# Optimization experiments

Measured on AMD Instinct MI355X. Metric: run time of the kernel, lower is better.

The kernel has to match this reference:

```python
import jax, jax.numpy as jnp
import numpy as np

B, S, E, H = 2, 2048, 1024, 16
DH = E // H  # 64


def setup_inputs() -> dict:
    key = jax.random.key(0)
    ks = jax.random.split(key, 9)
    sc = 1.0 / np.sqrt(E)
    return {
        "x": jax.random.normal(ks[0], (B, S, E), dtype=jnp.float32),
        "Wq": jax.random.normal(ks[1], (E, E), dtype=jnp.float32) * sc,
        "bq": jax.random.normal(ks[2], (E,), dtype=jnp.float32) * 0.02,
        "Wk": jax.random.normal(ks[3], (E, E), dtype=jnp.float32) * sc,
        "bk": jax.random.normal(ks[4], (E,), dtype=jnp.float32) * 0.02,
        "Wv": jax.random.normal(ks[5], (E, E), dtype=jnp.float32) * sc,
        "bv": jax.random.normal(ks[6], (E,), dtype=jnp.float32) * 0.02,
        "Wo": jax.random.normal(ks[7], (E, E), dtype=jnp.float32) * sc,
        "bo": jax.random.normal(ks[8], (E,), dtype=jnp.float32) * 0.02,
    }


def reference(x, Wq, bq, Wk, bk, Wv, bv, Wo, bo):
    b, s, e = x.shape
    h, dh = H, e // H
    # NOTE: original torch code does .view(B, H, S, Dh) on the [B, S, E]
    # projection WITHOUT transposing first; we replicate that exact reshape.
    q = (x @ Wq.T + bq).reshape(b, h, s, dh)
    k = (x @ Wk.T + bk).reshape(b, h, s, dh)
    v = (x @ Wv.T + bv).reshape(b, h, s, dh)
    scale = 1.0 / jnp.sqrt(jnp.asarray(dh, dtype=x.dtype))
    scores = jax.nn.softmax(jnp.einsum("bhqd,bhkd->bhqk", q, k) * scale, axis=-1)
    out = jnp.einsum("bhqk,bhkd->bhqd", scores, v)  # [B,H,S,Dh]
    out = out.transpose(0, 2, 1, 3).reshape(b, s, e)  # matches torch transpose(1,2).view
    return out @ Wo.T + bo
```

## Files before the change

### kernel.cpp

```cpp
#include <hip/hip_runtime.h>
#include <hip/hip_bf16.h>
#include <stdint.h>

typedef __bf16 bf16x8 __attribute__((ext_vector_type(8)));
typedef float  f32x4  __attribute__((ext_vector_type(4)));
typedef float  f32x16 __attribute__((ext_vector_type(16)));
typedef __hip_bfloat16 bf16;

__device__ __forceinline__ void gll16(const void* g, void* l) {
    typedef const unsigned int __attribute__((address_space(1)))* gp_t;
    typedef unsigned int __attribute__((address_space(3)))* lp_t;
    __builtin_amdgcn_global_load_lds((gp_t)(g), (lp_t)(l), 16, 0, 0);
}

__device__ __forceinline__ float fexp2(float x) {
#if __has_builtin(__builtin_amdgcn_exp2f)
    return __builtin_amdgcn_exp2f(x);
#else
    float r; asm volatile("v_exp_f32 %0, %1" : "=v"(r) : "v"(x)); return r;
#endif
}

__device__ __forceinline__ float tmax16(const f32x16& v) {
    float a0 = fmaxf(v[0], v[1]),   a1 = fmaxf(v[2], v[3]);
    float a2 = fmaxf(v[4], v[5]),   a3 = fmaxf(v[6], v[7]);
    float a4 = fmaxf(v[8], v[9]),   a5 = fmaxf(v[10], v[11]);
    float a6 = fmaxf(v[12], v[13]), a7 = fmaxf(v[14], v[15]);
    float b0 = fmaxf(a0, a1), b1 = fmaxf(a2, a3);
    float b2 = fmaxf(a4, a5), b3 = fmaxf(a6, a7);
    return fmaxf(fmaxf(b0, b1), fmaxf(b2, b3));
}
__device__ __forceinline__ float tsum16(const f32x16& v) {
    float a0 = v[0] + v[1],   a1 = v[2] + v[3];
    float a2 = v[4] + v[5],   a3 = v[6] + v[7];
    float a4 = v[8] + v[9],   a5 = v[10] + v[11];
    float a6 = v[12] + v[13], a7 = v[14] + v[15];
    float b0 = a0 + a1, b1 = a2 + a3, b2 = a4 + a5, b3 = a6 + a7;
    return (b0 + b1) + (b2 + b3);
}

__global__ __launch_bounds__(256) void prep_convert(
    const float* __restrict__ x,
    const float* __restrict__ wq, const float* __restrict__ wk,
    const float* __restrict__ wv, const float* __restrict__ wo,
    bf16* __restrict__ Xb, bf16* __restrict__ Wcat, bf16* __restrict__ Wob)
{
    int i = blockIdx.x * blockDim.x + threadIdx.x;
    int base = i * 4;
    const float* src; bf16* dst;
    if      (base < 4194304) { src = x  + base;             dst = Xb   + base; }
    else if (base < 5242880) { src = wq + (base - 4194304); dst = Wcat + (base - 4194304); }
    else if (base < 6291456) { src = wk + (base - 5242880); dst = Wcat + 1048576 + (base - 5242880); }
    else if (base < 7340032) { src = wv + (base - 6291456); dst = Wcat + 2097152 + (base - 6291456); }
    else                     { src = wo + (base - 7340032); dst = Wob  + (base - 7340032); }
    float4 v = *(const float4*)src;
    union { bf16 h[4]; ushort4 u; } cv;
    cv.h[0] = __float2bfloat16(v.x);
    cv.h[1] = __float2bfloat16(v.y);
    cv.h[2] = __float2bfloat16(v.z);
    cv.h[3] = __float2bfloat16(v.w);
    *(ushort4*)dst = cv.u;
}

__global__ __launch_bounds__(256, 2) void gemm_qkv(
    const bf16* __restrict__ X, const bf16* __restrict__ Wc,
    const float* __restrict__ bq, const float* __restrict__ bk, const float* __restrict__ bv,
    bf16* __restrict__ Pq, bf16* __restrict__ Pk, bf16* __restrict__ Pv)
{
    __shared__ __align__(16) bf16 Ab[128 * 32];
    __shared__ __align__(16) bf16 Bb[128 * 32];
    const int id = blockIdx.x;
    const int sid = (id & 7) * 96 + (id >> 3);
    const int t = threadIdx.x;
    const int lane = t & 63, w = t >> 6;
    const int lr = lane & 15, lg = lane >> 4;
    const int wr = w >> 1, wc = w & 1;
    const int row0 = (sid / 24) * 128, col0 = (sid % 24) * 128;

    f32x4 acc[4][4] = {};

    const char* Xc  = (const char*)X;
    const char* Wcc = (const char*)Wc;
    char* AbC = (char*)Ab;
    char* BbC = (char*)Bb;
    const int o0 = t * 16, o1 = o0 + 4096;
    const int ldsoff = w * 1024;

    for (int k0 = 0; k0 < 1024; k0 += 32) {
        __syncthreads();
        gll16(Xc  + (size_t)(row0 + (o0 >> 6)) * 2048 + (size_t)k0 * 2 + (o0 & 63), AbC + ldsoff);
        gll16(Wcc + (size_t)(col0 + (o0 >> 6)) * 2048 + (size_t)k0 * 2 + (o0 & 63), BbC + ldsoff);
        gll16(Xc  + (size_t)(row0 + (o1 >> 6)) * 2048 + (size_t)k0 * 2 + (o1 & 63), AbC + 4096 + ldsoff);
        gll16(Wcc + (size_t)(col0 + (o1 >> 6)) * 2048 + (size_t)k0 * 2 + (o1 & 63), BbC + 4096 + ldsoff);
        __syncthreads();
        bf16x8 af[4], bw[4];
        #pragma unroll
        for (int i = 0; i < 4; ++i)
            af[i] = *(const bf16x8*)(AbC + ((wr * 64 + i * 16 + lr) * 32 + lg * 8) * 2);
        #pragma unroll
        for (int j = 0; j < 4; ++j)
            bw[j] = *(const bf16x8*)(BbC + ((wc * 64 + j * 16 + lr) * 32 + lg * 8) * 2);
        #pragma unroll
        for (int i = 0; i < 4; ++i)
            #pragma unroll
            for (int j = 0; j < 4; ++j)
                acc[i][j] = __builtin_amdgcn_mfma_f32_16x16x32_bf16(af[i], bw[j], acc[i][j], 0, 0, 0);
    }

    const int mid = col0 >> 10;
    const float* bias = (mid == 0) ? bq : (mid == 1 ? bk : bv);
    bf16* Out = (mid == 0) ? Pq : (mid == 1 ? Pk : Pv);
    const float scale = (mid == 0) ? 0.125f * 1.44269504f : 1.0f;
    const int nc0 = col0 - (mid << 10) + wc * 64;
    const int mr0 = row0 + wr * 64;
    #pragma unroll
    for (int i = 0; i < 4; ++i)
        #pragma unroll
        for (int j = 0; j < 4; ++j) {
            int cc = nc0 + j * 16 + lr;
            float bsv = bias[cc];
            #pragma unroll
            for (int p = 0; p < 4; ++p) {
                int rr = mr0 + i * 16 + lg * 4 + p;
                Out[(size_t)rr * 1024 + cc] = __float2bfloat16((acc[i][j][p] + bsv) * scale);
            }
        }
}

__global__ __launch_bounds__(256) void transpose_v(const bf16* __restrict__ Pv, bf16* __restrict__ Vt)
{
    __shared__ bf16 tile[64][72];
    const int head = blockIdx.y;
    const int st   = blockIdx.x;
    const bf16* src = Pv + (size_t)head * 131072 + (size_t)st * 4096;
    bf16* dst = Vt + (size_t)head * 131072 + (size_t)st * 64;
    const int t = threadIdx.x;
    const int rr = t >> 2, c0 = (t & 3) * 16;
    #pragma unroll
    for (int u = 0; u < 2; ++u) {
        bf16x8 v = *(const bf16x8*)(src + rr * 64 + c0 + u * 8);
        #pragma unroll
        for (int e = 0; e < 8; ++e) tile[rr][c0 + u * 8 + e] = ((const bf16*)&v)[e];
    }
    __syncthreads();
    #pragma unroll
    for (int u = 0; u < 2; ++u) {
        bf16 ov[8];
        #pragma unroll
        for (int e = 0; e < 8; ++e) {
            int y = u * 8 + e;
            int z = (y & 3) | ((y & 8) >> 1) | ((y & 4) << 1);
            ov[e] = tile[c0 + z][rr];
        }
        *(bf16x8*)(dst + (size_t)rr * 2048 + c0 + u * 8) = *(const bf16x8*)ov;
    }
}

__global__ __launch_bounds__(512, 4) void attn_fwd(
    const bf16* __restrict__ Pq, const bf16* __restrict__ Pk,
    const bf16* __restrict__ Vt, bf16* __restrict__ Of)
{
    __shared__ __align__(16) bf16 Kl[2][128 * 64];
    __shared__ __align__(16) bf16 Vl[2][64 * 128];

    const int blk0 = blockIdx.x;
    const int blk = (blk0 & 7) * 64 + (blk0 >> 3);
    const int head = blk >> 4;
    const int qt = blk & 15;
    const int bb = head >> 4, hh = head & 15;
    const bf16* Qh = Pq + (size_t)head * 131072;
    const char* Khc = (const char*)(Pk + (size_t)head * 131072);
    const char* Vhc = (const char*)(Vt + (size_t)head * 131072);

    const int t = threadIdx.x;
    const int lane = t & 63, w = t >> 6;
    const int qg = w & 3, kh = w >> 2;
    const int ql = lane & 31, hi = lane >> 5;
    const int q0 = qt * 128 + qg * 32;

    bf16x8 qf[4];
    #pragma unroll
    for (int m = 0; m < 4; ++m)
        qf[m] = *(const bf16x8*)(Qh + (size_t)(q0 + ql) * 64 + m * 16 + hi * 8);

    f32x16 acc[2] = {};
    float m_run = -1e30f, l_run = 0.f;

    const int stg_key = t >> 3, stg_ks = t & 7;
    const int stg_d   = t >> 4, stg_vs = t & 15;
    const size_t kgo = (size_t)stg_key * 128 + ((stg_ks ^ (stg_key & 7)) * 16);
    const size_t vgo = (size_t)stg_d * 4096 + ((stg_vs ^ (stg_d & 7)) * 16);
    const int ldst = w * 1024;

#define STAGE(S0, BUF)                                                          \
    {                                                                           \
        char* KB = (char*)(Kl[BUF]);                                            \
        char* VB = (char*)(Vl[BUF]);                                            \
        _Pragma("unroll")                                                       \
        for (int qq = 0; qq < 2; ++qq) {                                        \
            gll16(Khc + (size_t)(S0) * 128 + (size_t)qq * 8192 + kgo,           \
                  KB + qq * 8192 + ldst);                                       \
            gll16(Vhc + (size_t)(S0) * 2 + (size_t)qq * 131072 + vgo,           \
                  VB + qq * 8192 + ldst);                                       \
        }                                                                       \
    }

    STAGE(0, 0);
    STAGE(128, 1);

    int cur = 0;
    for (int s0 = 0; s0 < 2048; s0 += 128) {
        if (s0 < 1920) {
            asm volatile("s_waitcnt vmcnt(4)\n\ts_barrier" ::: "memory");
        } else {
            asm volatile("s_waitcnt vmcnt(0)\n\ts_barrier" ::: "memory");
        }

        const char* KlC = (const char*)(Kl[cur]);
        const char* VlC = (const char*)(Vl[cur]);

        f32x16 sa[2] = {};
        __builtin_amdgcn_s_setprio(1);
        #pragma unroll
        for (int kb = 0; kb < 2; ++kb) {
            int row = kh * 64 + kb * 32 + ql;
            #pragma unroll
            for (int m = 0; m < 4; ++m) {
                int byt = row * 128 + ((32 * m + 16 * hi) ^ ((row & 7) << 4));
                bf16x8 kf = *(const bf16x8*)(KlC + byt);
                sa[kb] = __builtin_amdgcn_mfma_f32_32x32x16_bf16(kf, qf[m], sa[kb], 0, 0, 0);
            }
        }
        __builtin_amdgcn_s_setprio(0);

        float mx = fmaxf(tmax16(sa[0]), tmax16(sa[1]));
        mx = fmaxf(mx, __shfl_xor(mx, 32));

        float mn;
        if (__all(mx - m_run <= 8.0f)) {
            mn = m_run;
        } else {
            mn = fmaxf(m_run, mx);
            float al = fexp2(m_run - mn);
            m_run = mn;
            l_run *= al;
            #pragma unroll
            for (int r = 0; r < 16; ++r) { acc[0][r] *= al; acc[1][r] *= al; }
        }

        #pragma unroll
        for (int kb = 0; kb < 2; ++kb)
            #pragma unroll
            for (int r = 0; r < 16; ++r)
                sa[kb][r] = fexp2(sa[kb][r] - mn);
        float rs = tsum16(sa[0]) + tsum16(sa[1]);
        rs += __shfl_xor(rs, 32);
        l_run += rs;

        __builtin_amdgcn_s_setprio(1);
        #pragma unroll
        for (int sbl = 0; sbl < 4; ++sbl) {
            const int kb = sbl >> 1, par = (sbl & 1) * 8;
            const int sbg = kh * 4 + sbl;
            bf16x8 pa;
            #pragma unroll
            for (int e = 0; e < 8; ++e) pa[e] = (__bf16)sa[kb][par + e];
            #pragma unroll
            for (int db = 0; db < 2; ++db) {
                int row = db * 32 + ql;
                int byt = row * 256 + ((sbg * 32 + hi * 16) ^ ((row & 7) << 4));
                bf16x8 vf = *(const bf16x8*)(VlC + byt);
                acc[db] = __builtin_amdgcn_mfma_f32_32x32x16_bf16(vf, pa, acc[db], 0, 0, 0);
            }
        }
        __builtin_amdgcn_s_setprio(0);

        __builtin_amdgcn_s_barrier();
        if (s0 + 256 < 2048) STAGE(s0 + 256, cur);
        cur ^= 1;
    }
#undef STAGE

    float* cb1 = (float*)Kl;
    float* cb2 = (float*)Vl;
    const int idx = qg * 64 + lane;
    if (kh == 1) {
        #pragma unroll
        for (int r = 0; r < 16; ++r) cb1[idx * 18 + r] = acc[0][r];
        cb1[idx * 18 + 16] = m_run;
        cb1[idx * 18 + 17] = l_run;
        #pragma unroll
        for (int r = 0; r < 16; ++r) cb2[idx * 17 + r] = acc[1][r];
    }
    __syncthreads();
    if (kh == 0) {
        float m1 = cb1[idx * 18 + 16], l1 = cb1[idx * 18 + 17];
        float mN = fmaxf(m_run, m1);
        float a0 = fexp2(m_run - mN), a1 = fexp2(m1 - mN);
        float inv = 1.0f / (l_run * a0 + l1 * a1);
        bf16* orow = Of + (size_t)(bb * 2048 + q0 + ql) * 1024 + hh * 64;
        #pragma unroll
        for (int db = 0; db < 2; ++db)
            #pragma unroll
            for (int g = 0; g < 4; ++g) {
                union { bf16 h[4]; ushort4 u; } ob;
                #pragma unroll
                for (int j = 0; j < 4; ++j) {
                    int r = 4 * g + j;
                    float p1 = (db == 0) ? cb1[idx * 18 + r] : cb2[idx * 17 + r];
                    ob.h[j] = __float2bfloat16((acc[db][r] * a0 + p1 * a1) * inv);
                }
                *(ushort4*)(orow + db * 32 + 8 * g + 4 * hi) = ob.u;
            }
    }
}

__global__ __launch_bounds__(256, 2) void gemm_out(
    const bf16* __restrict__ A, const bf16* __restrict__ W,
    const float* __restrict__ bo, float* __restrict__ C)
{
    __shared__ __align__(16) bf16 Ab[128 * 32];
    __shared__ __align__(16) bf16 Bb[128 * 32];
    const int id = blockIdx.x;
    const int sid = (id & 7) * 32 + (id >> 3);
    const int t = threadIdx.x;
    const int lane = t & 63, w = t >> 6;
    const int lr = lane & 15, lg = lane >> 4;
    const int wr = w >> 1, wc = w & 1;
    const int row0 = (sid / 8) * 128, col0 = (sid % 8) * 128;

    f32x4 acc[4][4] = {};
    const char* Ac = (const char*)A;
    const char* Wc = (const char*)W;
    char* AbC = (char*)Ab;
    char* BbC = (char*)Bb;
    const int o0 = t * 16, o1 = o0 + 4096;
    const int ldsoff = w * 1024;

    for (int k0 = 0; k0 < 1024; k0 += 32) {
        __syncthreads();
        gll16(Ac + (size_t)(row0 + (o0 >> 6)) * 2048 + (size_t)k0 * 2 + (o0 & 63), AbC + ldsoff);
        gll16(Wc + (size_t)(col0 + (o0 >> 6)) * 2048 + (size_t)k0 * 2 + (o0 & 63), BbC + ldsoff);
        gll16(Ac + (size_t)(row0 + (o1 >> 6)) * 2048 + (size_t)k0 * 2 + (o1 & 63), AbC + 4096 + ldsoff);
        gll16(Wc + (size_t)(col0 + (o1 >> 6)) * 2048 + (size_t)k0 * 2 + (o1 & 63), BbC + 4096 + ldsoff);
        __syncthreads();
        bf16x8 af[4], bw[4];
        #pragma unroll
        for (int i = 0; i < 4; ++i)
            af[i] = *(const bf16x8*)(AbC + ((wr * 64 + i * 16 + lr) * 32 + lg * 8) * 2);
        #pragma unroll
        for (int j = 0; j < 4; ++j)
            bw[j] = *(const bf16x8*)(BbC + ((wc * 64 + j * 16 + lr) * 32 + lg * 8) * 2);
        #pragma unroll
        for (int i = 0; i < 4; ++i)
            #pragma unroll
            for (int j = 0; j < 4; ++j)
                acc[i][j] = __builtin_amdgcn_mfma_f32_16x16x32_bf16(af[i], bw[j], acc[i][j], 0, 0, 0);
    }

    const int nc0 = col0 + wc * 64;
    const int mr0 = row0 + wr * 64;
    #pragma unroll
    for (int i = 0; i < 4; ++i)
        #pragma unroll
        for (int j = 0; j < 4; ++j) {
            int cc = nc0 + j * 16 + lr;
            float bsv = bo[cc];
            #pragma unroll
            for (int p = 0; p < 4; ++p) {
                int rr = mr0 + i * 16 + lg * 4 + p;
                C[(size_t)rr * 1024 + cc] = acc[i][j][p] + bsv;
            }
        }
}

extern "C" void kernel_launch(void* const* d_in, const int* in_sizes, int n_in,
                              void* d_out, int out_size, void* d_ws, size_t ws_size,
                              hipStream_t stream) {
    const float* x  = (const float*)d_in[0];
    const float* Wq = (const float*)d_in[1];
    const float* bq = (const float*)d_in[2];
    const float* Wk = (const float*)d_in[3];
    const float* bk = (const float*)d_in[4];
    const float* Wv = (const float*)d_in[5];
    const float* bv = (const float*)d_in[6];
    const float* Wo = (const float*)d_in[7];
    const float* bo = (const float*)d_in[8];
    float* out = (float*)d_out;

    char* ws = (char*)d_ws;
    bf16* Xb   = (bf16*)(ws + 0);
    bf16* Wcat = (bf16*)(ws + 8388608);
    bf16* Wob  = (bf16*)(ws + 14680064);
    bf16* Pq   = (bf16*)(ws + 16777216);
    bf16* Pk   = (bf16*)(ws + 25165824);
    bf16* Pv   = (bf16*)(ws + 33554432);
    bf16* Vt   = (bf16*)(ws + 0);
    bf16* Of   = (bf16*)(ws + 33554432);
    (void)ws_size; (void)in_sizes; (void)n_in; (void)out_size;

    prep_convert<<<8192, 256, 0, stream>>>(x, Wq, Wk, Wv, Wo, Xb, Wcat, Wob);
    gemm_qkv<<<768, 256, 0, stream>>>(Xb, Wcat, bq, bk, bv, Pq, Pk, Pv);
    transpose_v<<<dim3(32, 32), 256, 0, stream>>>(Pv, Vt);
    attn_fwd<<<512, 512, 0, stream>>>(Pq, Pk, Vt, Of);
    gemm_out<<<256, 256, 0, stream>>>(Of, Wob, bo, out);
}
```

Before: 122.9 us.

## Software-pipeline attention loop so next QK^T overlaps current softmax and PV

After: 131.4 us. +6.9%, slower.

```diff
diff --git a/kernel.cpp b/kernel.cpp
--- a/kernel.cpp
+++ b/kernel.cpp
@@ -156,7 +156,7 @@
     }
 }
 
-__global__ __launch_bounds__(512, 4) void attn_fwd(
+__global__ __launch_bounds__(512, 2) void attn_fwd(
     const bf16* __restrict__ Pq, const bf16* __restrict__ Pk,
     const bf16* __restrict__ Vt, bf16* __restrict__ Of)
 {
@@ -183,7 +183,9 @@
     for (int m = 0; m < 4; ++m)
         qf[m] = *(const bf16x8*)(Qh + (size_t)(q0 + ql) * 64 + m * 16 + hi * 8);
 
+    f32x16 zz = {};
     f32x16 acc[2] = {};
+    f32x16 saA[2], saB[2];
     float m_run = -1e30f, l_run = 0.f;
 
     const int stg_key = t >> 3, stg_ks = t & 7;
@@ -192,95 +194,105 @@
     const size_t vgo = (size_t)stg_d * 4096 + ((stg_vs ^ (stg_d & 7)) * 16);
     const int ldst = w * 1024;
 
-#define STAGE(S0, BUF)                                                          \
+#define STAGE(KEY0, BUF)                                                        \
     {                                                                           \
         char* KB = (char*)(Kl[BUF]);                                            \
         char* VB = (char*)(Vl[BUF]);                                            \
         _Pragma("unroll")                                                       \
         for (int qq = 0; qq < 2; ++qq) {                                        \
-            gll16(Khc + (size_t)(S0) * 128 + (size_t)qq * 8192 + kgo,           \
+            gll16(Khc + (size_t)(KEY0) * 128 + (size_t)qq * 8192 + kgo,         \
                   KB + qq * 8192 + ldst);                                       \
-            gll16(Vhc + (size_t)(S0) * 2 + (size_t)qq * 131072 + vgo,           \
+            gll16(Vhc + (size_t)(KEY0) * 2 + (size_t)qq * 131072 + vgo,         \
                   VB + qq * 8192 + ldst);                                       \
         }                                                                       \
     }
 
+#define QK_STEP(SA, KBUF)                                                       \
+    {                                                                           \
+        const char* KlC_ = (const char*)(Kl[KBUF]);                             \
+        SA[0] = zz; SA[1] = zz;                                                 \
+        _Pragma("unroll")                                                       \
+        for (int kb = 0; kb < 2; ++kb) {                                        \
+            int row = kh * 64 + kb * 32 + ql;                                   \
+            _Pragma("unroll")                                                   \
+            for (int m = 0; m < 4; ++m) {                                       \
+                int byt = row * 128 + ((32 * m + 16 * hi) ^ ((row & 7) << 4));  \
+                bf16x8 kf = *(const bf16x8*)(KlC_ + byt);                       \
+                SA[kb] = __builtin_amdgcn_mfma_f32_32x32x16_bf16(kf, qf[m], SA[kb], 0, 0, 0); \
+            }                                                                   \
+        }                                                                       \
+    }
+
+#define SM_PV(SA, VBUF)                                                         \
+    {                                                                           \
+        float mx = fmaxf(tmax16(SA[0]), tmax16(SA[1]));                         \
+        mx = fmaxf(mx, __shfl_xor(mx, 32));                                     \
+        float mn;                                                               \
+        if (__all(mx - m_run <= 8.0f)) {                                        \
+            mn = m_run;                                                         \
+        } else {                                                                \
+            mn = fmaxf(m_run, mx);                                              \
+            float al = fexp2(m_run - mn);                                       \
+            m_run = mn; l_run *= al;                                            \
+            _Pragma("unroll")                                                   \
+            for (int r = 0; r < 16; ++r) { acc[0][r] *= al; acc[1][r] *= al; }  \
+        }                                                                       \
+        _Pragma("unroll")                                                       \
+        for (int kb = 0; kb < 2; ++kb)                                          \
+            _Pragma("unroll")                                                   \
+            for (int r = 0; r < 16; ++r) SA[kb][r] = fexp2(SA[kb][r] - mn);     \
+        float rs = tsum16(SA[0]) + tsum16(SA[1]);                               \
+        rs += __shfl_xor(rs, 32);                                               \
+        l_run += rs;                                                            \
+        const char* VlC_ = (const char*)(Vl[VBUF]);                             \
+        __builtin_amdgcn_s_setprio(1);                                          \
+        _Pragma("unroll")                                                       \
+        for (int sbl = 0; sbl < 4; ++sbl) {                                     \
+            const int kb = sbl >> 1, par = (sbl & 1) * 8;                       \
+            const int sbg = kh * 4 + sbl;                                       \
+            bf16x8 pa;                                                          \
+            _Pragma("unroll")                                                   \
+            for (int e = 0; e < 8; ++e) pa[e] = (__bf16)SA[kb][par + e];        \
+            _Pragma("unroll")                                                   \
+            for (int db = 0; db < 2; ++db) {                                    \
+                int row = db * 32 + ql;                                         \
+                int byt = row * 256 + ((sbg * 32 + hi * 16) ^ ((row & 7) << 4));\
+                bf16x8 vf = *(const bf16x8*)(VlC_ + byt);                       \
+                acc[db] = __builtin_amdgcn_mfma_f32_32x32x16_bf16(vf, pa, acc[db], 0, 0, 0); \
+            }                                                                   \
+        }                                                                       \
+        __builtin_amdgcn_s_setprio(0);                                          \
+    }
+
     STAGE(0, 0);
     STAGE(128, 1);
-
-    int cur = 0;
-    for (int s0 = 0; s0 < 2048; s0 += 128) {
-        if (s0 < 1920) {
-            asm volatile("s_waitcnt vmcnt(4)\n\ts_barrier" ::: "memory");
-        } else {
-            asm volatile("s_waitcnt vmcnt(0)\n\ts_barrier" ::: "memory");
-        }
-
-        const char* KlC = (const char*)(Kl[cur]);
-        const char* VlC = (const char*)(Vl[cur]);
-
-        f32x16 sa[2] = {};
-        __builtin_amdgcn_s_setprio(1);
-        #pragma unroll
-        for (int kb = 0; kb < 2; ++kb) {
-            int row = kh * 64 + kb * 32 + ql;
-            #pragma unroll
-            for (int m = 0; m < 4; ++m) {
-                int byt = row * 128 + ((32 * m + 16 * hi) ^ ((row & 7) << 4));
-                bf16x8 kf = *(const bf16x8*)(KlC + byt);
-                sa[kb] = __builtin_amdgcn_mfma_f32_32x32x16_bf16(kf, qf[m], sa[kb], 0, 0, 0);
-            }
-        }
-        __builtin_amdgcn_s_setprio(0);
-
-        float mx = fmaxf(tmax16(sa[0]), tmax16(sa[1]));
-        mx = fmaxf(mx, __shfl_xor(mx, 32));
-
-        float mn;
-        if (__all(mx - m_run <= 8.0f)) {
-            mn = m_run;
-        } else {
-            mn = fmaxf(m_run, mx);
-            float al = fexp2(m_run - mn);
-            m_run = mn;
-            l_run *= al;
-            #pragma unroll
-            for (int r = 0; r < 16; ++r) { acc[0][r] *= al; acc[1][r] *= al; }
-        }
-
-        #pragma unroll
-        for (int kb = 0; kb < 2; ++kb)
-            #pragma unroll
-            for (int r = 0; r < 16; ++r)
-                sa[kb][r] = fexp2(sa[kb][r] - mn);
-        float rs = tsum16(sa[0]) + tsum16(sa[1]);
-        rs += __shfl_xor(rs, 32);
-        l_run += rs;
-
-        __builtin_amdgcn_s_setprio(1);
-        #pragma unroll
-        for (int sbl = 0; sbl < 4; ++sbl) {
-            const int kb = sbl >> 1, par = (sbl & 1) * 8;
-            const int sbg = kh * 4 + sbl;
-            bf16x8 pa;
-            #pragma unroll
-            for (int e = 0; e < 8; ++e) pa[e] = (__bf16)sa[kb][par + e];
-            #pragma unroll
-            for (int db = 0; db < 2; ++db) {
-                int row = db * 32 + ql;
-                int byt = row * 256 + ((sbg * 32 + hi * 16) ^ ((row & 7) << 4));
-                bf16x8 vf = *(const bf16x8*)(VlC + byt);
-                acc[db] = __builtin_amdgcn_mfma_f32_32x32x16_bf16(vf, pa, acc[db], 0, 0, 0);
-            }
-        }
-        __builtin_amdgcn_s_setprio(0);
-
+    asm volatile("s_waitcnt vmcnt(4)\n\ts_barrier" ::: "memory");
+    QK_STEP(saA, 0);
+
+    #pragma unroll 1
+    for (int t2 = 0; t2 < 7; ++t2) {
+        const int tt = t2 * 2;
+        asm volatile("s_waitcnt vmcnt(0)\n\ts_barrier" ::: "memory");
+        QK_STEP(saB, 1);
+        SM_PV(saA, 0);
         __builtin_amdgcn_s_barrier();
-        if (s0 + 256 < 2048) STAGE(s0 + 256, cur);
-        cur ^= 1;
-    }
+        STAGE((tt + 2) * 128, 0);
+        asm volatile("s_waitcnt vmcnt(0)\n\ts_barrier" ::: "memory");
+        QK_STEP(saA, 0);
+        SM_PV(saB, 1);
+        __builtin_amdgcn_s_barrier();
+        STAGE((tt + 3) * 128, 1);
+    }
+
+    asm volatile("s_waitcnt vmcnt(0)\n\ts_barrier" ::: "memory");
+    QK_STEP(saB, 1);
+    SM_PV(saA, 0);
+    SM_PV(saB, 1);
 #undef STAGE
-
+#undef QK_STEP
+#undef SM_PV
+
+    __syncthreads();
     float* cb1 = (float*)Kl;
     float* cb2 = (float*)Vl;
     const int idx = qg * 64 + lane;
```
